# Kernel optimization log

Measured on AMD Instinct MI355X. Metric: run time of the kernel, lower is better.

Reference implementation:

```python
import jax, jax.numpy as jnp
import numpy as np

N_SRC = 100000   # source nodes (columns of adj)
N_DST = 50000    # target nodes (rows of adj)
N_EDGES = 3200000
N_IN = 256
N_OUT = 128


def setup_inputs() -> dict:
    key = jax.random.key(0)
    k = jax.random.split(key, 7)
    stdv = 1.0 / np.sqrt(N_IN)
    x = jax.random.normal(k[0], (N_SRC, N_IN), dtype=jnp.float32)
    W = jax.random.uniform(k[1], (N_OUT, N_IN), minval=-stdv, maxval=stdv, dtype=jnp.float32)
    b = jax.random.uniform(k[2], (N_OUT,), minval=-stdv, maxval=stdv, dtype=jnp.float32)
    adj_rows = jax.random.randint(k[3], (N_EDGES,), 0, N_DST)
    adj_cols = jax.random.randint(k[4], (N_EDGES,), 0, N_SRC)
    # mean-aggregation-style normalized weights (generic positive values)
    adj_vals = jax.random.uniform(k[5], (N_EDGES,), dtype=jnp.float32)
    previous_index = jax.random.randint(k[6], (N_DST,), 0, N_SRC)
    return {"x": x, "W": W, "b": b, "adj_vals": adj_vals,
            "adj_rows": adj_rows, "adj_cols": adj_cols,
            "previous_index": previous_index}


def reference(x, W, b, adj_vals, adj_rows, adj_cols, previous_index):
    # linear projection: h = x @ W.T + b            -> [N_SRC, n_out]
    h = jnp.einsum('ni,oi->no', x, W) + b
    # spmm(adj, h) via COO gather + segment-sum      -> [N_DST, n_out]
    msgs = adj_vals[:, None] * h[adj_cols]          # [E, n_out]
    support = jax.ops.segment_sum(msgs, adj_rows, num_segments=previous_index.shape[0])
    # gather self features and concat                -> [N_DST, 2*n_out]
    return jnp.concatenate([h[previous_index], support], axis=1)
```

## Files before the change

kernel.cpp:

```cpp
#include <hip/hip_runtime.h>
#include <hip/hip_bf16.h>

#define N_IN      256
#define N_OUTC    128
#define RPS       64
#define RPS_SHIFT 6
#define NSB_MAX   1024
#define TILE      4096
#define EPT       16
#define SPILL_CAP 8192

typedef __attribute__((ext_vector_type(8))) short bf16x8;
typedef __attribute__((ext_vector_type(4))) float f32x4;
typedef unsigned short ushort_t;
typedef unsigned int uint_t;

__device__ inline unsigned short f2bf(float f) {
    unsigned u = __float_as_uint(f);
    unsigned r = u + 0x7fffu + ((u >> 16) & 1u);
    return (unsigned short)(r >> 16);
}
__device__ inline float bf_lo(uint_t g) { return __uint_as_float(g << 16); }
__device__ inline float bf_hi(uint_t g) { return __uint_as_float(g & 0xFFFF0000u); }

__global__ void cvtW_kernel(const float* __restrict__ W, ushort_t* __restrict__ wb, int n) {
    int i = blockIdx.x * blockDim.x + threadIdx.x;
    if (i < n) wb[i] = f2bf(W[i]);
}

__global__ __launch_bounds__(256) void fused_build_gemm_kernel(
        const int* __restrict__ rows, const int* __restrict__ cols,
        const float* __restrict__ vals, int E,
        int* __restrict__ sbCount, int2* __restrict__ sbList, int sbCap, int nsb,
        int* __restrict__ spillCnt, int4* __restrict__ spill, int nbBuild,
        const float* __restrict__ x, const ushort_t* __restrict__ wb,
        const float* __restrict__ b, ushort_t* __restrict__ h16) {
    __shared__ int cur[NSB_MAX];
    __shared__ int gbase[NSB_MAX];
    const int tid = threadIdx.x;

    if (blockIdx.x < (uint_t)nbBuild) {
        const int base = blockIdx.x * TILE;
        for (int i = tid; i < nsb; i += 256) cur[i] = 0;
        __syncthreads();

        int ex[EPT], evb[EPT], esb[EPT], erk[EPT];
        #pragma unroll
        for (int k = 0; k < EPT; k++) {
            int e = base + tid + k * 256;
            if (e < E) {
                int r = rows[e], c = cols[e];
                evb[k] = __float_as_int(vals[e]);
                esb[k] = r >> RPS_SHIFT;
                ex[k]  = c | ((r & (RPS - 1)) << 17);
                erk[k] = atomicAdd(&cur[esb[k]], 1);
            } else esb[k] = -1;
        }
        __syncthreads();
        for (int i = tid; i < nsb; i += 256)
            gbase[i] = cur[i] ? atomicAdd(&sbCount[i], cur[i]) : 0;
        __syncthreads();

        #pragma unroll
        for (int k = 0; k < EPT; k++) {
            if (esb[k] < 0) continue;
            int pos = gbase[esb[k]] + erk[k];
            if (pos < sbCap) {
                sbList[(size_t)esb[k] * sbCap + pos] = make_int2(ex[k], evb[k]);
            } else {
                int sp = atomicAdd(spillCnt, 1);
                if (sp < SPILL_CAP)
                    spill[sp] = make_int4((esb[k] << RPS_SHIFT) + (int)(((uint_t)ex[k]) >> 17),
                                          ex[k] & 0x1FFFF, evb[k], 0);
            }
        }
        return;
    }

    const int blk  = blockIdx.x - nbBuild;
    const int wave = tid >> 6;
    const int lane = tid & 63;
    const int quad = lane >> 4;
    const int l16  = lane & 15;
    const int m0   = blk * 16;
    const int colbase = wave * 32;

    f32x4 acc0 = {0.f, 0.f, 0.f, 0.f};
    f32x4 acc1 = {0.f, 0.f, 0.f, 0.f};

    const float* xrow = x + (size_t)(m0 + l16) * N_IN + quad * 8;
    const ushort_t* w0 = wb + (size_t)(colbase + l16) * N_IN + quad * 8;
    const ushort_t* w1 = w0 + 16 * N_IN;

    #pragma unroll
    for (int kb = 0; kb < N_IN; kb += 32) {
        float4 a0 = *(const float4*)(xrow + kb);
        float4 a1 = *(const float4*)(xrow + kb + 4);
        union { bf16x8 v; __hip_bfloat162 h2[4]; } u;
        u.h2[0] = __float22bfloat162_rn(make_float2(a0.x, a0.y));
        u.h2[1] = __float22bfloat162_rn(make_float2(a0.z, a0.w));
        u.h2[2] = __float22bfloat162_rn(make_float2(a1.x, a1.y));
        u.h2[3] = __float22bfloat162_rn(make_float2(a1.z, a1.w));
        bf16x8 bf0 = *(const bf16x8*)(w0 + kb);
        bf16x8 bf1 = *(const bf16x8*)(w1 + kb);
        acc0 = __builtin_amdgcn_mfma_f32_16x16x32_bf16(u.v, bf0, acc0, 0, 0, 0);
        acc1 = __builtin_amdgcn_mfma_f32_16x16x32_bf16(u.v, bf1, acc1, 0, 0, 0);
    }

    const int c0 = colbase + l16;
    const int c1 = c0 + 16;
    const float bv0 = b[c0];
    const float bv1 = b[c1];
    ushort_t* hp = h16 + (size_t)(m0 + quad * 4) * N_OUTC;
    #pragma unroll
    for (int r = 0; r < 4; r++) {
        hp[(size_t)r * N_OUTC + c0] = f2bf(acc0[r] + bv0);
        hp[(size_t)r * N_OUTC + c1] = f2bf(acc1[r] + bv1);
    }
}

__global__ __launch_bounds__(1024) void sbscan_kernel(const int* __restrict__ sbCount, int sbCap,
                                                      int* __restrict__ sbBase, int nsb) {
    __shared__ int a[NSB_MAX], bsh[NSB_MAX];
    int tid = threadIdx.x;
    int v = 0;
    if (tid < nsb) { v = sbCount[tid]; if (v > sbCap) v = sbCap; }
    a[tid] = v; __syncthreads();
    int* src = a; int* dst = bsh;
    for (int off = 1; off < 1024; off <<= 1) {
        dst[tid] = src[tid] + ((tid >= off) ? src[tid - off] : 0);
        __syncthreads();
        int* t = src; src = dst; dst = t;
    }
    if (tid < nsb) sbBase[tid] = tid ? src[tid - 1] : 0;
}

__global__ __launch_bounds__(256) void sort_kernel(const int* __restrict__ sbCount,
                                                   const int* __restrict__ sbBase,
                                                   const int2* __restrict__ sbList, int sbCap,
                                                   int2* __restrict__ csr,
                                                   int* __restrict__ rowStart, int* __restrict__ rowCnt,
                                                   int Ndst) {
    __shared__ int hist[RPS];
    __shared__ int scanA[RPS];
    __shared__ int curx[RPS];
    const int sb  = blockIdx.x;
    const int tid = threadIdx.x;
    int len = sbCount[sb]; if (len > sbCap) len = sbCap;
    const int base = sbBase[sb];
    const int2* lp = sbList + (size_t)sb * sbCap;

    if (tid < RPS) hist[tid] = 0;
    __syncthreads();

    int i = tid;
    for (; i + 768 < len; i += 1024) {
        int x0 = lp[i].x, x1 = lp[i + 256].x, x2 = lp[i + 512].x, x3 = lp[i + 768].x;
        atomicAdd(&hist[((uint_t)x0) >> 17], 1);
        atomicAdd(&hist[((uint_t)x1) >> 17], 1);
        atomicAdd(&hist[((uint_t)x2) >> 17], 1);
        atomicAdd(&hist[((uint_t)x3) >> 17], 1);
    }
    for (; i < len; i += 256) atomicAdd(&hist[((uint_t)lp[i].x) >> 17], 1);
    __syncthreads();

    if (tid < RPS) scanA[tid] = hist[tid];
    __syncthreads();
    for (int off = 1; off < RPS; off <<= 1) {
        int t = 0;
        if (tid < RPS) t = scanA[tid] + ((tid >= off) ? scanA[tid - off] : 0);
        __syncthreads();
        if (tid < RPS) scanA[tid] = t;
        __syncthreads();
    }
    if (tid < RPS) {
        int excl = tid ? scanA[tid - 1] : 0;
        curx[tid] = excl;
        int r = sb * RPS + tid;
        if (r < Ndst) { rowStart[r] = base + excl; rowCnt[r] = hist[tid]; }
    }
    __syncthreads();

    i = tid;
    for (; i + 768 < len; i += 1024) {
        int2 e0 = lp[i], e1 = lp[i + 256], e2 = lp[i + 512], e3 = lp[i + 768];
        int p0 = atomicAdd(&curx[((uint_t)e0.x) >> 17], 1);
        int p1 = atomicAdd(&curx[((uint_t)e1.x) >> 17], 1);
        int p2 = atomicAdd(&curx[((uint_t)e2.x) >> 17], 1);
        int p3 = atomicAdd(&curx[((uint_t)e3.x) >> 17], 1);
        csr[(size_t)base + p0] = make_int2(e0.x & 0x1FFFF, e0.y);
        csr[(size_t)base + p1] = make_int2(e1.x & 0x1FFFF, e1.y);
        csr[(size_t)base + p2] = make_int2(e2.x & 0x1FFFF, e2.y);
        csr[(size_t)base + p3] = make_int2(e3.x & 0x1FFFF, e3.y);
    }
    for (; i < len; i += 256) {
        int2 e = lp[i];
        int pos = atomicAdd(&curx[((uint_t)e.x) >> 17], 1);
        csr[(size_t)base + pos] = make_int2(e.x & 0x1FFFF, e.y);
    }
}

__global__ __launch_bounds__(256) void spmm_concat_kernel(const ushort_t* __restrict__ h16,
                                                          const int* __restrict__ rowStart,
                                                          const int* __restrict__ rowCnt,
                                                          const int2* __restrict__ csr,
                                                          const int* __restrict__ prev,
                                                          float* __restrict__ out, int Ndst) {
    int r = blockIdx.x * 4 + (threadIdx.x >> 6);
    if (r >= Ndst) return;
    const int lane = threadIdx.x & 63;
    const int cnt = rowCnt[r];
    const int2* bk = csr + rowStart[r];

    float2 acc = {0.f, 0.f};
    for (int bse = 0; bse < cnt; bse += 64) {
        int idx = bse + lane;
        int2 my = make_int2(0, 0);
        if (idx < cnt) my = bk[idx];
        int m = cnt - bse; if (m > 64) m = 64;
        int mg = (m + 7) & ~7;
        for (int j = 0; j < mg; j += 8) {
            int c0 = __shfl(my.x, j + 0), c1 = __shfl(my.x, j + 1);
            int c2 = __shfl(my.x, j + 2), c3 = __shfl(my.x, j + 3);
            int c4 = __shfl(my.x, j + 4), c5 = __shfl(my.x, j + 5);
            int c6 = __shfl(my.x, j + 6), c7 = __shfl(my.x, j + 7);
            uint_t g0 = *(const uint_t*)(h16 + (size_t)c0 * N_OUTC + 2 * lane);
            uint_t g1 = *(const uint_t*)(h16 + (size_t)c1 * N_OUTC + 2 * lane);
            uint_t g2 = *(const uint_t*)(h16 + (size_t)c2 * N_OUTC + 2 * lane);
            uint_t g3 = *(const uint_t*)(h16 + (size_t)c3 * N_OUTC + 2 * lane);
            uint_t g4 = *(const uint_t*)(h16 + (size_t)c4 * N_OUTC + 2 * lane);
            uint_t g5 = *(const uint_t*)(h16 + (size_t)c5 * N_OUTC + 2 * lane);
            uint_t g6 = *(const uint_t*)(h16 + (size_t)c6 * N_OUTC + 2 * lane);
            uint_t g7 = *(const uint_t*)(h16 + (size_t)c7 * N_OUTC + 2 * lane);
            float v0 = __int_as_float(__shfl(my.y, j + 0));
            float v1 = __int_as_float(__shfl(my.y, j + 1));
            float v2 = __int_as_float(__shfl(my.y, j + 2));
            float v3 = __int_as_float(__shfl(my.y, j + 3));
            float v4 = __int_as_float(__shfl(my.y, j + 4));
            float v5 = __int_as_float(__shfl(my.y, j + 5));
            float v6 = __int_as_float(__shfl(my.y, j + 6));
            float v7 = __int_as_float(__shfl(my.y, j + 7));
            acc.x += v0 * bf_lo(g0); acc.y += v0 * bf_hi(g0);
            acc.x += v1 * bf_lo(g1); acc.y += v1 * bf_hi(g1);
            acc.x += v2 * bf_lo(g2); acc.y += v2 * bf_hi(g2);
            acc.x += v3 * bf_lo(g3); acc.y += v3 * bf_hi(g3);
            acc.x += v4 * bf_lo(g4); acc.y += v4 * bf_hi(g4);
            acc.x += v5 * bf_lo(g5); acc.y += v5 * bf_hi(g5);
            acc.x += v6 * bf_lo(g6); acc.y += v6 * bf_hi(g6);
            acc.x += v7 * bf_lo(g7); acc.y += v7 * bf_hi(g7);
        }
    }

    int p = prev[r];
    uint_t g = *(const uint_t*)(h16 + (size_t)p * N_OUTC + 2 * lane);
    float2* o = (float2*)(out + (size_t)r * 256);
    o[lane]      = make_float2(bf_lo(g), bf_hi(g));
    o[64 + lane] = make_float2(acc.x, acc.y);
}

__global__ void spill_kernel(const ushort_t* __restrict__ h16, const int4* __restrict__ spill,
                             const int* __restrict__ spillCnt, float* __restrict__ out) {
    int n = *spillCnt; if (n > SPILL_CAP) n = SPILL_CAP;
    int total = n * 64;
    for (int t = blockIdx.x * blockDim.x + threadIdx.x; t < total; t += gridDim.x * blockDim.x) {
        int idx = t >> 6, lane = t & 63;
        int4 s = spill[idx];
        uint_t g = *(const uint_t*)(h16 + (size_t)s.y * N_OUTC + 2 * lane);
        float v = __int_as_float(s.z);
        atomicAdd(&out[(size_t)s.x * 256 + 128 + 2 * lane],     v * bf_lo(g));
        atomicAdd(&out[(size_t)s.x * 256 + 128 + 2 * lane + 1], v * bf_hi(g));
    }
}

__global__ __launch_bounds__(256) void gemm_only_kernel(const float* __restrict__ x,
                                                        const ushort_t* __restrict__ wb,
                                                        const float* __restrict__ b,
                                                        ushort_t* __restrict__ h16) {
    const int tid  = threadIdx.x;
    const int wave = tid >> 6;
    const int lane = tid & 63;
    const int quad = lane >> 4;
    const int l16  = lane & 15;
    const int m0   = blockIdx.x * 16;
    const int colbase = wave * 32;
    f32x4 acc0 = {0.f, 0.f, 0.f, 0.f};
    f32x4 acc1 = {0.f, 0.f, 0.f, 0.f};
    const float* xrow = x + (size_t)(m0 + l16) * N_IN + quad * 8;
    const ushort_t* w0 = wb + (size_t)(colbase + l16) * N_IN + quad * 8;
    const ushort_t* w1 = w0 + 16 * N_IN;
    #pragma unroll
    for (int kb = 0; kb < N_IN; kb += 32) {
        float4 a0 = *(const float4*)(xrow + kb);
        float4 a1 = *(const float4*)(xrow + kb + 4);
        union { bf16x8 v; __hip_bfloat162 h2[4]; } u;
        u.h2[0] = __float22bfloat162_rn(make_float2(a0.x, a0.y));
        u.h2[1] = __float22bfloat162_rn(make_float2(a0.z, a0.w));
        u.h2[2] = __float22bfloat162_rn(make_float2(a1.x, a1.y));
        u.h2[3] = __float22bfloat162_rn(make_float2(a1.z, a1.w));
        bf16x8 bf0 = *(const bf16x8*)(w0 + kb);
        bf16x8 bf1 = *(const bf16x8*)(w1 + kb);
        acc0 = __builtin_amdgcn_mfma_f32_16x16x32_bf16(u.v, bf0, acc0, 0, 0, 0);
        acc1 = __builtin_amdgcn_mfma_f32_16x16x32_bf16(u.v, bf1, acc1, 0, 0, 0);
    }
    const int c0 = colbase + l16;
    const int c1 = c0 + 16;
    const float bv0 = b[c0];
    const float bv1 = b[c1];
    ushort_t* hp = h16 + (size_t)(m0 + quad * 4) * N_OUTC;
    #pragma unroll
    for (int r = 0; r < 4; r++) {
        hp[(size_t)r * N_OUTC + c0] = f2bf(acc0[r] + bv0);
        hp[(size_t)r * N_OUTC + c1] = f2bf(acc1[r] + bv1);
    }
}

__global__ void concat_only_kernel(const ushort_t* __restrict__ h16, const int* __restrict__ prev,
                                   float* __restrict__ out, int Ndst) {
    int t = blockIdx.x * blockDim.x + threadIdx.x;
    int r = t >> 6, lane = t & 63;
    if (r >= Ndst) return;
    uint_t g = *(const uint_t*)(h16 + (size_t)prev[r] * N_OUTC + 2 * lane);
    ((float2*)out)[(size_t)r * 128 + lane] = make_float2(bf_lo(g), bf_hi(g));
}

__global__ void spmm_atomic_kernel(const ushort_t* __restrict__ h16, const int* __restrict__ rows,
                                   const int* __restrict__ cols, const float* __restrict__ vals,
                                   int E, float* __restrict__ out) {
    long long t = (long long)blockIdx.x * blockDim.x + threadIdx.x;
    int e = (int)(t >> 6), lane = (int)(t & 63);
    if (e >= E) return;
    uint_t g = *(const uint_t*)(h16 + (size_t)cols[e] * N_OUTC + 2 * lane);
    float v = vals[e];
    int r = rows[e];
    atomicAdd(&out[(size_t)r * 256 + 128 + 2 * lane],     v * bf_lo(g));
    atomicAdd(&out[(size_t)r * 256 + 128 + 2 * lane + 1], v * bf_hi(g));
}

extern "C" void kernel_launch(void* const* d_in, const int* in_sizes, int n_in,
                              void* d_out, int out_size, void* d_ws, size_t ws_size,
                              hipStream_t stream) {
    const float* x    = (const float*)d_in[0];
    const float* W    = (const float*)d_in[1];
    const float* b    = (const float*)d_in[2];
    const float* vals = (const float*)d_in[3];
    const int*   rows = (const int*)d_in[4];
    const int*   cols = (const int*)d_in[5];
    const int*   prev = (const int*)d_in[6];
    float* out = (float*)d_out;

    const int Nsrc = in_sizes[0] / N_IN;
    const int E    = in_sizes[3];
    const int Ndst = in_sizes[6];
    const int NSB  = (Ndst + RPS - 1) / RPS;
    const int sbCap = E / NSB + 516;
    const int nbBuild = (E + TILE - 1) / TILE;
    const int gemmBlocks = Nsrc / 16;

    char* ws = (char*)d_ws;
    size_t off = 0;
    ushort_t* h16 = (ushort_t*)(ws + off);
    off += (size_t)Nsrc * N_OUTC * sizeof(ushort_t);
    ushort_t* wb = (ushort_t*)(ws + off);
    off += (size_t)N_OUTC * N_IN * sizeof(ushort_t);
    off = (off + 255) & ~(size_t)255;
    int* sbCount  = (int*)(ws + off);
    int* spillCnt = sbCount + NSB;
    size_t memsetBytes = ((size_t)NSB + 1) * sizeof(int);
    off += memsetBytes;
    off = (off + 255) & ~(size_t)255;
    int* sbBase = (int*)(ws + off);
    off += (size_t)NSB * sizeof(int);
    off = (off + 255) & ~(size_t)255;
    int* rowStart = (int*)(ws + off);
    off += (size_t)Ndst * sizeof(int);
    int* rowCnt = (int*)(ws + off);
    off += (size_t)Ndst * sizeof(int);
    off = (off + 255) & ~(size_t)255;
    int4* spill = (int4*)(ws + off);
    off += (size_t)SPILL_CAP * sizeof(int4);
    off = (off + 255) & ~(size_t)255;
    int2* sbList = (int2*)(ws + off);
    off += (size_t)NSB * sbCap * sizeof(int2);
    off = (off + 255) & ~(size_t)255;
    int2* csr = (int2*)(ws + off);
    off += (size_t)E * sizeof(int2);

    cvtW_kernel<<<(N_OUTC * N_IN + 255) / 256, 256, 0, stream>>>(W, wb, N_OUTC * N_IN);

    if (off <= ws_size && NSB <= NSB_MAX) {
        hipMemsetAsync(sbCount, 0, memsetBytes, stream);
        fused_build_gemm_kernel<<<nbBuild + gemmBlocks, 256, 0, stream>>>(
            rows, cols, vals, E, sbCount, sbList, sbCap, NSB, spillCnt, spill, nbBuild,
            x, wb, b, h16);
        sbscan_kernel<<<1, 1024, 0, stream>>>(sbCount, sbCap, sbBase, NSB);
        sort_kernel<<<NSB, 256, 0, stream>>>(sbCount, sbBase, sbList, sbCap,
                                             csr, rowStart, rowCnt, Ndst);
        spmm_concat_kernel<<<(Ndst + 3) / 4, 256, 0, stream>>>(h16, rowStart, rowCnt, csr,
                                                               prev, out, Ndst);
        spill_kernel<<<64, 256, 0, stream>>>(h16, spill, spillCnt, out);
    } else {
        gemm_only_kernel<<<gemmBlocks, 256, 0, stream>>>(x, wb, b, h16);
        hipMemsetAsync(out, 0, (size_t)out_size * sizeof(float), stream);
        concat_only_kernel<<<((size_t)Ndst * 64 + 255) / 256, 256, 0, stream>>>(h16, prev, out, Ndst);
        spmm_atomic_kernel<<<((size_t)E * 64 + 255) / 256, 256, 0, stream>>>(h16, rows, cols, vals, E, out);
    }
}
```

Baseline: 437.2 us.

## Replace superblock bucket sort with global row histogram, scan, and atomic scatter

Replaces the two-level CSR build (superblock bucketing with spill list, per-superblock local sort) with a direct counting sort. A per-row histogram is folded into the GEMM blocks, a single-block scan turns the counts into row offsets, and a scatter kernel places each edge with a global atomic on its row cursor. This removes the intermediate sbList buffer, the extra sort pass and the spill handling. In exchange it issues 3.2M global atomics over 50K rows twice, and edge order within each row becomes nondeterministic.

```diff
diff --git a/kernel.cpp b/kernel.cpp
--- a/kernel.cpp
+++ b/kernel.cpp
@@ -1,14 +1,9 @@
 #include <hip/hip_runtime.h>
 #include <hip/hip_bf16.h>
 
-#define N_IN      256
-#define N_OUTC    128
-#define RPS       64
-#define RPS_SHIFT 6
-#define NSB_MAX   1024
-#define TILE      4096
-#define EPT       16
-#define SPILL_CAP 8192
+#define N_IN   256
+#define N_OUTC 128
+#define SC_EPT 8
 
 typedef __attribute__((ext_vector_type(8))) short bf16x8;
 typedef __attribute__((ext_vector_type(4))) float f32x4;
@@ -28,61 +23,24 @@
     if (i < n) wb[i] = f2bf(W[i]);
 }
 
-__global__ __launch_bounds__(256) void fused_build_gemm_kernel(
-        const int* __restrict__ rows, const int* __restrict__ cols,
-        const float* __restrict__ vals, int E,
-        int* __restrict__ sbCount, int2* __restrict__ sbList, int sbCap, int nsb,
-        int* __restrict__ spillCnt, int4* __restrict__ spill, int nbBuild,
+__global__ __launch_bounds__(256) void fused_hist_gemm_kernel(
+        const int* __restrict__ rows, int E, int histPerBlock, int* __restrict__ rowCnt,
         const float* __restrict__ x, const ushort_t* __restrict__ wb,
         const float* __restrict__ b, ushort_t* __restrict__ h16) {
-    __shared__ int cur[NSB_MAX];
-    __shared__ int gbase[NSB_MAX];
     const int tid = threadIdx.x;
 
-    if (blockIdx.x < (uint_t)nbBuild) {
-        const int base = blockIdx.x * TILE;
-        for (int i = tid; i < nsb; i += 256) cur[i] = 0;
-        __syncthreads();
-
-        int ex[EPT], evb[EPT], esb[EPT], erk[EPT];
-        #pragma unroll
-        for (int k = 0; k < EPT; k++) {
-            int e = base + tid + k * 256;
-            if (e < E) {
-                int r = rows[e], c = cols[e];
-                evb[k] = __float_as_int(vals[e]);
-                esb[k] = r >> RPS_SHIFT;
-                ex[k]  = c | ((r & (RPS - 1)) << 17);
-                erk[k] = atomicAdd(&cur[esb[k]], 1);
-            } else esb[k] = -1;
-        }
-        __syncthreads();
-        for (int i = tid; i < nsb; i += 256)
-            gbase[i] = cur[i] ? atomicAdd(&sbCount[i], cur[i]) : 0;
-        __syncthreads();
-
-        #pragma unroll
-        for (int k = 0; k < EPT; k++) {
-            if (esb[k] < 0) continue;
-            int pos = gbase[esb[k]] + erk[k];
-            if (pos < sbCap) {
-                sbList[(size_t)esb[k] * sbCap + pos] = make_int2(ex[k], evb[k]);
-            } else {
-                int sp = atomicAdd(spillCnt, 1);
-                if (sp < SPILL_CAP)
-                    spill[sp] = make_int4((esb[k] << RPS_SHIFT) + (int)(((uint_t)ex[k]) >> 17),
-                                          ex[k] & 0x1FFFF, evb[k], 0);
-            }
-        }
-        return;
-    }
-
-    const int blk  = blockIdx.x - nbBuild;
+    {
+        int e0 = blockIdx.x * histPerBlock;
+        int e1 = e0 + histPerBlock; if (e1 > E) e1 = E;
+        for (int e = e0 + tid; e < e1; e += 256)
+            atomicAdd(&rowCnt[rows[e]], 1);
+    }
+
     const int wave = tid >> 6;
     const int lane = tid & 63;
     const int quad = lane >> 4;
     const int l16  = lane & 15;
-    const int m0   = blk * 16;
+    const int m0   = blockIdx.x * 16;
     const int colbase = wave * 32;
 
     f32x4 acc0 = {0.f, 0.f, 0.f, 0.f};
@@ -119,84 +77,52 @@
     }
 }
 
-__global__ __launch_bounds__(1024) void sbscan_kernel(const int* __restrict__ sbCount, int sbCap,
-                                                      int* __restrict__ sbBase, int nsb) {
-    __shared__ int a[NSB_MAX], bsh[NSB_MAX];
-    int tid = threadIdx.x;
-    int v = 0;
-    if (tid < nsb) { v = sbCount[tid]; if (v > sbCap) v = sbCap; }
-    a[tid] = v; __syncthreads();
+__global__ __launch_bounds__(1024) void scan_kernel(const int* __restrict__ rowCnt,
+                                                    int* __restrict__ rowStart,
+                                                    int* __restrict__ rowFill, int Ndst) {
+    __shared__ int a[1024], bsh[1024];
+    const int tid = threadIdx.x;
+    const int npt = (Ndst + 1023) >> 10;
+    const int base = tid * npt;
+    int s = 0;
+    for (int i = 0; i < npt; i++) {
+        int idx = base + i;
+        if (idx < Ndst) s += rowCnt[idx];
+    }
+    a[tid] = s; __syncthreads();
     int* src = a; int* dst = bsh;
     for (int off = 1; off < 1024; off <<= 1) {
         dst[tid] = src[tid] + ((tid >= off) ? src[tid - off] : 0);
         __syncthreads();
         int* t = src; src = dst; dst = t;
     }
-    if (tid < nsb) sbBase[tid] = tid ? src[tid - 1] : 0;
-}
-
-__global__ __launch_bounds__(256) void sort_kernel(const int* __restrict__ sbCount,
-                                                   const int* __restrict__ sbBase,
-                                                   const int2* __restrict__ sbList, int sbCap,
-                                                   int2* __restrict__ csr,
-                                                   int* __restrict__ rowStart, int* __restrict__ rowCnt,
-                                                   int Ndst) {
-    __shared__ int hist[RPS];
-    __shared__ int scanA[RPS];
-    __shared__ int curx[RPS];
-    const int sb  = blockIdx.x;
-    const int tid = threadIdx.x;
-    int len = sbCount[sb]; if (len > sbCap) len = sbCap;
-    const int base = sbBase[sb];
-    const int2* lp = sbList + (size_t)sb * sbCap;
-
-    if (tid < RPS) hist[tid] = 0;
-    __syncthreads();
-
-    int i = tid;
-    for (; i + 768 < len; i += 1024) {
-        int x0 = lp[i].x, x1 = lp[i + 256].x, x2 = lp[i + 512].x, x3 = lp[i + 768].x;
-        atomicAdd(&hist[((uint_t)x0) >> 17], 1);
-        atomicAdd(&hist[((uint_t)x1) >> 17], 1);
-        atomicAdd(&hist[((uint_t)x2) >> 17], 1);
-        atomicAdd(&hist[((uint_t)x3) >> 17], 1);
-    }
-    for (; i < len; i += 256) atomicAdd(&hist[((uint_t)lp[i].x) >> 17], 1);
-    __syncthreads();
-
-    if (tid < RPS) scanA[tid] = hist[tid];
-    __syncthreads();
-    for (int off = 1; off < RPS; off <<= 1) {
-        int t = 0;
-        if (tid < RPS) t = scanA[tid] + ((tid >= off) ? scanA[tid - off] : 0);
-        __syncthreads();
-        if (tid < RPS) scanA[tid] = t;
-        __syncthreads();
-    }
-    if (tid < RPS) {
-        int excl = tid ? scanA[tid - 1] : 0;
-        curx[tid] = excl;
-        int r = sb * RPS + tid;
-        if (r < Ndst) { rowStart[r] = base + excl; rowCnt[r] = hist[tid]; }
-    }
-    __syncthreads();
-
-    i = tid;
-    for (; i + 768 < len; i += 1024) {
-        int2 e0 = lp[i], e1 = lp[i + 256], e2 = lp[i + 512], e3 = lp[i + 768];
-        int p0 = atomicAdd(&curx[((uint_t)e0.x) >> 17], 1);
-        int p1 = atomicAdd(&curx[((uint_t)e1.x) >> 17], 1);
-        int p2 = atomicAdd(&curx[((uint_t)e2.x) >> 17], 1);
-        int p3 = atomicAdd(&curx[((uint_t)e3.x) >> 17], 1);
-        csr[(size_t)base + p0] = make_int2(e0.x & 0x1FFFF, e0.y);
-        csr[(size_t)base + p1] = make_int2(e1.x & 0x1FFFF, e1.y);
-        csr[(size_t)base + p2] = make_int2(e2.x & 0x1FFFF, e2.y);
-        csr[(size_t)base + p3] = make_int2(e3.x & 0x1FFFF, e3.y);
-    }
-    for (; i < len; i += 256) {
-        int2 e = lp[i];
-        int pos = atomicAdd(&curx[((uint_t)e.x) >> 17], 1);
-        csr[(size_t)base + pos] = make_int2(e.x & 0x1FFFF, e.y);
+    int run = tid ? src[tid - 1] : 0;
+    for (int i = 0; i < npt; i++) {
+        int idx = base + i;
+        if (idx < Ndst) {
+            rowStart[idx] = run;
+            rowFill[idx]  = run;
+            run += rowCnt[idx];
+        }
+    }
+}
+
+__global__ __launch_bounds__(256) void scatter_kernel(const int* __restrict__ rows,
+                                                      const int* __restrict__ cols,
+                                                      const float* __restrict__ vals, int E,
+                                                      int* __restrict__ rowFill,
+                                                      int2* __restrict__ csr) {
+    const int base = blockIdx.x * (256 * SC_EPT) + threadIdx.x;
+    #pragma unroll
+    for (int k = 0; k < SC_EPT; k++) {
+        int e = base + k * 256;
+        if (e < E) {
+            int r = rows[e];
+            int c = cols[e];
+            float v = vals[e];
+            int pos = atomicAdd(&rowFill[r], 1);
+            csr[pos] = make_int2(c, __float_as_int(v));
+        }
     }
 }
 
@@ -258,20 +184,6 @@
     o[64 + lane] = make_float2(acc.x, acc.y);
 }
 
-__global__ void spill_kernel(const ushort_t* __restrict__ h16, const int4* __restrict__ spill,
-                             const int* __restrict__ spillCnt, float* __restrict__ out) {
-    int n = *spillCnt; if (n > SPILL_CAP) n = SPILL_CAP;
-    int total = n * 64;
-    for (int t = blockIdx.x * blockDim.x + threadIdx.x; t < total; t += gridDim.x * blockDim.x) {
-        int idx = t >> 6, lane = t & 63;
-        int4 s = spill[idx];
-        uint_t g = *(const uint_t*)(h16 + (size_t)s.y * N_OUTC + 2 * lane);
-        float v = __int_as_float(s.z);
-        atomicAdd(&out[(size_t)s.x * 256 + 128 + 2 * lane],     v * bf_lo(g));
-        atomicAdd(&out[(size_t)s.x * 256 + 128 + 2 * lane + 1], v * bf_hi(g));
-    }
-}
-
 __global__ __launch_bounds__(256) void gemm_only_kernel(const float* __restrict__ x,
                                                         const ushort_t* __restrict__ wb,
                                                         const float* __restrict__ b,
@@ -351,10 +263,9 @@
     const int Nsrc = in_sizes[0] / N_IN;
     const int E    = in_sizes[3];
     const int Ndst = in_sizes[6];
-    const int NSB  = (Ndst + RPS - 1) / RPS;
-    const int sbCap = E / NSB + 516;
-    const int nbBuild = (E + TILE - 1) / TILE;
     const int gemmBlocks = Nsrc / 16;
+    const int histPerBlock = (E + gemmBlocks - 1) / gemmBlocks;
+    const int scBlocks = (E + 256 * SC_EPT - 1) / (256 * SC_EPT);
 
     char* ws = (char*)d_ws;
     size_t off = 0;
@@ -363,41 +274,28 @@
     ushort_t* wb = (ushort_t*)(ws + off);
     off += (size_t)N_OUTC * N_IN * sizeof(ushort_t);
     off = (off + 255) & ~(size_t)255;
-    int* sbCount  = (int*)(ws + off);
-    int* spillCnt = sbCount + NSB;
-    size_t memsetBytes = ((size_t)NSB + 1) * sizeof(int);
+    int* rowCnt = (int*)(ws + off);
+    size_t memsetBytes = (size_t)Ndst * sizeof(int);
     off += memsetBytes;
-    off = (off + 255) & ~(size_t)255;
-    int* sbBase = (int*)(ws + off);
-    off += (size_t)NSB * sizeof(int);
     off = (off + 255) & ~(size_t)255;
     int* rowStart = (int*)(ws + off);
     off += (size_t)Ndst * sizeof(int);
-    int* rowCnt = (int*)(ws + off);
+    int* rowFill = (int*)(ws + off);
     off += (size_t)Ndst * sizeof(int);
-    off = (off + 255) & ~(size_t)255;
-    int4* spill = (int4*)(ws + off);
-    off += (size_t)SPILL_CAP * sizeof(int4);
-    off = (off + 255) & ~(size_t)255;
-    int2* sbList = (int2*)(ws + off);
-    off += (size_t)NSB * sbCap * sizeof(int2);
     off = (off + 255) & ~(size_t)255;
     int2* csr = (int2*)(ws + off);
     off += (size_t)E * sizeof(int2);
 
     cvtW_kernel<<<(N_OUTC * N_IN + 255) / 256, 256, 0, stream>>>(W, wb, N_OUTC * N_IN);
 
-    if (off <= ws_size && NSB <= NSB_MAX) {
-        hipMemsetAsync(sbCount, 0, memsetBytes, stream);
-        fused_build_gemm_kernel<<<nbBuild + gemmBlocks, 256, 0, stream>>>(
-            rows, cols, vals, E, sbCount, sbList, sbCap, NSB, spillCnt, spill, nbBuild,
-            x, wb, b, h16);
-        sbscan_kernel<<<1, 1024, 0, stream>>>(sbCount, sbCap, sbBase, NSB);
-        sort_kernel<<<NSB, 256, 0, stream>>>(sbCount, sbBase, sbList, sbCap,
-                                             csr, rowStart, rowCnt, Ndst);
+    if (off <= ws_size) {
+        hipMemsetAsync(rowCnt, 0, memsetBytes, stream);
+        fused_hist_gemm_kernel<<<gemmBlocks, 256, 0, stream>>>(
+            rows, E, histPerBlock, rowCnt, x, wb, b, h16);
+        scan_kernel<<<1, 1024, 0, stream>>>(rowCnt, rowStart, rowFill, Ndst);
+        scatter_kernel<<<scBlocks, 256, 0, stream>>>(rows, cols, vals, E, rowFill, csr);
         spmm_concat_kernel<<<(Ndst + 3) / 4, 256, 0, stream>>>(h16, rowStart, rowCnt, csr,
                                                                prev, out, Ndst);
-        spill_kernel<<<64, 256, 0, stream>>>(h16, spill, spillCnt, out);
     } else {
         gemm_only_kernel<<<gemmBlocks, 256, 0, stream>>>(x, wb, b, h16);
         hipMemsetAsync(out, 0, (size_t)out_size * sizeof(float), stream);
```

Result: slower. 813.0 us (+86.0%).
